# Kernel optimization log

Measured on AMD Instinct MI355X. Metric: run time of the kernel, lower is better.

The kernel has to match this reference:

```python
import jax, jax.numpy as jnp
import numpy as np

B, C, T = 2, 32, 7680
IN_CAPS = 122240  # ((7680-9+1)//4 - 9 + 1) * 2 * 32
OUT_CAPS, OUT_DIM, IN_DIM = 16, 16, 8
ROUTINGS = 3
DN = ('NCHW', 'OIHW', 'NCHW')


def squash(s, axis=-1):
    norm = jnp.linalg.norm(s, axis=axis, keepdims=True)
    scale = norm ** 2 / (1.0 + norm ** 2) / (norm + 1e-8)
    return scale * s


def setup_inputs() -> dict:
    key = jax.random.key(0)
    ks = jax.random.split(key, 9)
    return {
        'x': jax.random.normal(ks[0], (B, C, T), jnp.float32),
        'W_lin': jax.random.normal(ks[1], (C, C), jnp.float32) * 0.1,
        'b_lin': jnp.zeros((C,), jnp.float32),
        'W_conv1': jax.random.normal(ks[2], (16, 1, 1, 9), jnp.float32) * 0.1,
        'b_conv1': jnp.zeros((16,), jnp.float32),
        'W_conv2': jax.random.normal(ks[3], (16, 16, 1, 9), jnp.float32) * 0.05,
        'b_conv2': jnp.zeros((16,), jnp.float32),
        'W_caps': jax.random.normal(ks[4], (OUT_CAPS, IN_CAPS, OUT_DIM, IN_DIM), jnp.float32) * 0.01,
        'W_fc': jax.random.normal(ks[5], (1, 16, 16), jnp.float32) * 0.1,
        'b_fc': jnp.zeros((1,), jnp.float32),
    }


def reference(x, W_lin, b_lin, W_conv1, b_conv1, W_conv2, b_conv2, W_caps, W_fc, b_fc):
    # channel attention: shared linear applied to max-pool and avg-pool over time
    mx = x.max(axis=-1)                      # [B, C]
    av = x.mean(axis=-1)                     # [B, C]
    attn = jax.nn.sigmoid((mx @ W_lin.T + b_lin) + (av @ W_lin.T + b_lin))
    x = x * attn[:, :, None]                 # [B, C, T]

    # conv_first: Conv2d(1,16,(1,9),stride=(1,2)) + ELU + AvgPool2d((1,2),(1,2))
    h = x[:, None, :, :]                     # [B, 1, C, T]
    h = jax.lax.conv_general_dilated(h, W_conv1, (1, 2), 'VALID', dimension_numbers=DN)
    h = jax.nn.elu(h + b_conv1[None, :, None, None])   # [B, 16, 32, 3836]
    b_, ch, hh, ww = h.shape
    h = h[..., : (ww // 2) * 2].reshape(b_, ch, hh, ww // 2, 2).mean(-1)  # [B,16,32,1918]

    # primary capsules: Conv2d(16,16,(1,9)) -> reshape to [B, IN_CAPS, 8] -> squash
    h = jax.lax.conv_general_dilated(h, W_conv2, (1, 1), 'VALID', dimension_numbers=DN)
    h = h + b_conv2[None, :, None, None]     # [B, 16, 32, 1910]
    u = squash(h.reshape(b_, -1, IN_DIM))    # [B, 122240, 8]

    # dense capsule: x_hat[b,j,n,p] = sum_d W_caps[j,n,p,d] * u[b,n,d]
    x_hat = jnp.einsum('jnpd,bnd->bjnp', W_caps, u)  # [B, 16, 122240, 16]
    x_hat_det = jax.lax.stop_gradient(x_hat)
    b_logits = jnp.zeros((b_, OUT_CAPS, IN_CAPS), x_hat.dtype)
    v = None
    for i in range(ROUTINGS):
        c = jax.nn.softmax(b_logits, axis=1)             # [B, 16, 122240]
        xh = x_hat if i == ROUTINGS - 1 else x_hat_det
        v = squash(jnp.einsum('bjn,bjnp->bjp', c, xh))   # [B, 16, 16]
        if i < ROUTINGS - 1:
            b_logits = b_logits + jnp.einsum('bjp,bjnp->bjn', v, x_hat_det)

    # fc: Conv1d(16, 1, 16) over [B, 16, 16] -> [B, 1, 1] -> sigmoid -> squeeze
    out = jax.nn.sigmoid(jnp.einsum('bct,oct->bo', v, W_fc) + b_fc)
    return jnp.squeeze(out)                  # [B]
```

## Files before the change

### kernel.cpp

```cpp
#include <hip/hip_runtime.h>
#include <math.h>

#define IN_CAPS 122240
#define T_LEN   7680
#define PW      1918
#define HW      1910

#define OFF_MX    0
#define OFF_AV    64
#define OFF_ATTN  128
#define OFF_S0    192
#define OFF_S1    704
#define OFF_S2    1216
#define OFF_V0    1728
#define OFF_VSUM  2240
#define OFF_P     2816
#define OFF_H     1966848
#define OFF_U     3922688
#define OFF_XHAT  5878528

__global__ void k_rowstat(const float* __restrict__ x, float* __restrict__ ws) {
    int row = blockIdx.x;
    const float* xr = x + (size_t)row * T_LEN;
    float mx = -INFINITY, sm = 0.f;
    for (int i = threadIdx.x; i < T_LEN; i += 256) {
        float v = xr[i];
        mx = fmaxf(mx, v);
        sm += v;
    }
    __shared__ float smx[256], ssm[256];
    smx[threadIdx.x] = mx; ssm[threadIdx.x] = sm;
    __syncthreads();
    for (int s = 128; s > 0; s >>= 1) {
        if (threadIdx.x < s) {
            smx[threadIdx.x] = fmaxf(smx[threadIdx.x], smx[threadIdx.x + s]);
            ssm[threadIdx.x] += ssm[threadIdx.x + s];
        }
        __syncthreads();
    }
    if (threadIdx.x == 0) {
        ws[OFF_MX + row] = smx[0];
        ws[OFF_AV + row] = ssm[0] * (1.f / (float)T_LEN);
    }
}

__global__ void k_attn_zero(const float* __restrict__ Wl, const float* __restrict__ bl,
                            float* __restrict__ ws) {
    int t = threadIdx.x;
    for (int i = t; i < 1536; i += 256) ws[OFF_S0 + i] = 0.f;
    if (t < 64) {
        int b = t >> 5, c = t & 31;
        float acc = 2.f * bl[c];
        for (int k = 0; k < 32; k++)
            acc += (ws[OFF_MX + b * 32 + k] + ws[OFF_AV + b * 32 + k]) * Wl[c * 32 + k];
        ws[OFF_ATTN + t] = 1.f / (1.f + expf(-acc));
    }
}

__global__ void k_conv1pool(const float* __restrict__ x, const float* __restrict__ w1,
                            const float* __restrict__ b1, float* __restrict__ ws) {
    int idx = blockIdx.x * 256 + threadIdx.x;
    int w2 = idx % PW;
    int hh = (idx / PW) & 31;
    int oc = (idx / (PW * 32)) & 15;
    int b  = idx / (PW * 32 * 16);
    float a = ws[OFF_ATTN + b * 32 + hh];
    const float* xr = x + ((size_t)b * 32 + hh) * T_LEN + 4 * w2;
    const float* wk = w1 + oc * 9;
    float xv[11];
    #pragma unroll
    for (int k = 0; k < 11; k++) xv[k] = xr[k] * a;
    float o0 = 0.f, o1 = 0.f;
    #pragma unroll
    for (int k = 0; k < 9; k++) { o0 += wk[k] * xv[k]; o1 += wk[k] * xv[k + 2]; }
    o0 += b1[oc]; o1 += b1[oc];
    o0 = o0 > 0.f ? o0 : expm1f(o0);
    o1 = o1 > 0.f ? o1 : expm1f(o1);
    ws[OFF_P + idx] = 0.5f * (o0 + o1);
}

__global__ void k_conv2(const float* __restrict__ w2, const float* __restrict__ b2,
                        float* __restrict__ ws) {
    int idx = blockIdx.x * 256 + threadIdx.x;
    int w3 = idx % HW;
    int hh = (idx / HW) & 31;
    int oc = (idx / (HW * 32)) & 15;
    int b  = idx / (HW * 32 * 16);
    float acc = b2[oc];
    const float* wrow = w2 + oc * 144;
    const float* pb = ws + OFF_P + (size_t)b * 16 * 32 * PW + hh * PW + w3;
    #pragma unroll 4
    for (int ic = 0; ic < 16; ic++) {
        const float* pr = pb + (size_t)ic * 32 * PW;
        #pragma unroll
        for (int k = 0; k < 9; k++) acc += wrow[ic * 9 + k] * pr[k];
    }
    ws[OFF_H + idx] = acc;
}

__global__ void k_squash_u(float* __restrict__ ws) {
    int n = blockIdx.x * 256 + threadIdx.x;
    const float4* hp = (const float4*)(ws + OFF_H) + (size_t)n * 2;
    float4 a = hp[0], b = hp[1];
    float ns = a.x*a.x + a.y*a.y + a.z*a.z + a.w*a.w
             + b.x*b.x + b.y*b.y + b.z*b.z + b.w*b.w;
    float nrm = sqrtf(ns);
    float scale = ns / (1.f + ns) / (nrm + 1e-8f);
    a.x *= scale; a.y *= scale; a.z *= scale; a.w *= scale;
    b.x *= scale; b.y *= scale; b.z *= scale; b.w *= scale;
    float4* up = (float4*)(ws + OFF_U) + (size_t)n * 2;
    up[0] = a; up[1] = b;
}

__global__ void __launch_bounds__(256) k_xhat(const float* __restrict__ Wc,
                                              float* __restrict__ ws) {
    const int j = threadIdx.x >> 4;
    const int p = threadIdx.x & 15;
    const int n0 = blockIdx.x * 128;
    const float* u = ws + OFF_U;
    float* xhat = ws + OFF_XHAT;
    const size_t wbase = (size_t)j * IN_CAPS * 128 + (size_t)p * 8;
    float sum0 = 0.f, sum1 = 0.f;
    for (int k = 0; k < 128; k++) {
        const int n = n0 + k;
        const float4* wp = (const float4*)(Wc + wbase + (size_t)n * 128);
        float4 wa = wp[0], wb = wp[1];
        const float4* ua = (const float4*)(u + ((size_t)n << 3));
        const float4* ub = (const float4*)(u + ((size_t)(IN_CAPS + n) << 3));
        float4 a0 = ua[0], a1 = ua[1];
        float4 c0 = ub[0], c1 = ub[1];
        float xh0 = wa.x*a0.x + wa.y*a0.y + wa.z*a0.z + wa.w*a0.w
                  + wb.x*a1.x + wb.y*a1.y + wb.z*a1.z + wb.w*a1.w;
        float xh1 = wa.x*c0.x + wa.y*c0.y + wa.z*c0.z + wa.w*c0.w
                  + wb.x*c1.x + wb.y*c1.y + wb.z*c1.z + wb.w*c1.w;
        xhat[((size_t)n << 8) + (j << 4) + p] = xh0;
        xhat[((size_t)(IN_CAPS + n) << 8) + (j << 4) + p] = xh1;
        sum0 += xh0; sum1 += xh1;
    }
    atomicAdd(&ws[OFF_S0 + (j << 4) + p], sum0);
    atomicAdd(&ws[OFF_S0 + 256 + (j << 4) + p], sum1);
}

__global__ void __launch_bounds__(256) k_route(const float* __restrict__ xhat,
                                               const float* __restrict__ vin,
                                               float* __restrict__ sout,
                                               int nwaves_per_b) {
    const int tid = threadIdx.x;
    const int wid = tid >> 6;
    const int lane = tid & 63;
    const int j = lane >> 2;
    const int pq = lane & 3;
    const int b = wid & 1;
    __shared__ float vsh[512];
    for (int i = tid; i < 512; i += 256) vsh[i] = vin[i];
    __syncthreads();
    const float* vp = &vsh[(((b << 4) + j) << 4) + (pq << 2)];
    const float v0 = vp[0], v1 = vp[1], v2 = vp[2], v3 = vp[3];
    const int wb = (blockIdx.x << 1) + (wid >> 1);
    const float* xb = xhat + (size_t)b * IN_CAPS * 256;
    float4 acc = make_float4(0.f, 0.f, 0.f, 0.f);
    for (int n = wb; n < IN_CAPS; n += nwaves_per_b) {
        float4 xh = *(const float4*)(xb + ((size_t)n << 8) + (j << 4) + (pq << 2));
        float t = v0 * xh.x + v1 * xh.y + v2 * xh.z + v3 * xh.w;
        t += __shfl_xor(t, 1);
        t += __shfl_xor(t, 2);
        float tmax = t;
        tmax = fmaxf(tmax, __shfl_xor(tmax, 4));
        tmax = fmaxf(tmax, __shfl_xor(tmax, 8));
        tmax = fmaxf(tmax, __shfl_xor(tmax, 16));
        tmax = fmaxf(tmax, __shfl_xor(tmax, 32));
        float e = expf(t - tmax);
        float es = e;
        es += __shfl_xor(es, 4);
        es += __shfl_xor(es, 8);
        es += __shfl_xor(es, 16);
        es += __shfl_xor(es, 32);
        float c = e / es;
        acc.x += c * xh.x; acc.y += c * xh.y; acc.z += c * xh.z; acc.w += c * xh.w;
    }
    __shared__ float4 accsh[4][64];
    accsh[wid][lane] = acc;
    __syncthreads();
    if (tid < 128) {
        float4 a = accsh[wid][lane];
        float4 c = accsh[wid + 2][lane];
        float* dst = sout + (((wid << 4) + j) << 4) + (pq << 2);
        atomicAdd(dst + 0, a.x + c.x);
        atomicAdd(dst + 1, a.y + c.y);
        atomicAdd(dst + 2, a.z + c.z);
        atomicAdd(dst + 3, a.w + c.w);
    }
}

__global__ void __launch_bounds__(512) k_vstep(float* __restrict__ ws,
                                               const float* __restrict__ wfc,
                                               const float* __restrict__ bfc,
                                               float* __restrict__ out,
                                               int mode) {
    __shared__ float sv[512];
    const int t = threadIdx.x;
    int soff = (mode == 0) ? OFF_S0 : (mode == 1) ? OFF_S1 : OFF_S2;
    float val = ws[soff + t];
    if (mode == 0) val *= (1.f / 16.f);
    sv[t] = val;
    __syncthreads();
    const int bj = t >> 4;
    float ns = 0.f;
    #pragma unroll
    for (int p = 0; p < 16; p++) { float q = sv[(bj << 4) + p]; ns += q * q; }
    float nrm = sqrtf(ns);
    float scale = ns / (1.f + ns) / (nrm + 1e-8f);
    float v = scale * val;
    if (mode == 0) {
        ws[OFF_V0 + t] = v;
    } else if (mode == 1) {
        ws[OFF_VSUM + t] = ws[OFF_V0 + t] + v;
    } else {
        __syncthreads();
        sv[t] = v * wfc[t & 255];
        __syncthreads();
        for (int s = 128; s > 0; s >>= 1) {
            if ((t & 255) < s) sv[t] += sv[t + s];
            __syncthreads();
        }
        if ((t & 255) == 0)
            out[t >> 8] = 1.f / (1.f + expf(-(sv[t] + bfc[0])));
    }
}

extern "C" void kernel_launch(void* const* d_in, const int* in_sizes, int n_in,
                              void* d_out, int out_size, void* d_ws, size_t ws_size,
                              hipStream_t stream) {
    const float* x   = (const float*)d_in[0];
    const float* Wl  = (const float*)d_in[1];
    const float* bl  = (const float*)d_in[2];
    const float* W1  = (const float*)d_in[3];
    const float* b1  = (const float*)d_in[4];
    const float* W2  = (const float*)d_in[5];
    const float* b2  = (const float*)d_in[6];
    const float* Wc  = (const float*)d_in[7];
    const float* Wfc = (const float*)d_in[8];
    const float* bfc = (const float*)d_in[9];
    float* out = (float*)d_out;
    float* ws  = (float*)d_ws;

    k_rowstat  <<<64, 256, 0, stream>>>(x, ws);
    k_attn_zero<<<1, 256, 0, stream>>>(Wl, bl, ws);
    k_conv1pool<<<7672, 256, 0, stream>>>(x, W1, b1, ws);
    k_conv2    <<<7640, 256, 0, stream>>>(W2, b2, ws);
    k_squash_u <<<955, 256, 0, stream>>>(ws);
    k_xhat     <<<955, 256, 0, stream>>>(Wc, ws);
    k_vstep    <<<1, 512, 0, stream>>>(ws, Wfc, bfc, out, 0);
    k_route    <<<256, 256, 0, stream>>>(ws + OFF_XHAT, ws + OFF_V0, ws + OFF_S1, 512);
    k_vstep    <<<1, 512, 0, stream>>>(ws, Wfc, bfc, out, 1);
    k_route    <<<256, 256, 0, stream>>>(ws + OFF_XHAT, ws + OFF_VSUM, ws + OFF_S2, 512);
    k_vstep    <<<1, 512, 0, stream>>>(ws, Wfc, bfc, out, 2);
}
```

Before: 1.806 ms.

## Store x_hat in bf16 and restructure routing to one capsule per thread group

x_hat is now written as bf16 in the dense-capsule kernel and read back as bf16 in both routing passes, halving the bytes of the largest intermediate (about 500 MB in fp32). The routing kernel is rewritten so each group of 4 threads handles all 16 output capsules of one input capsule. The softmax over j then runs in registers instead of through cross-lane shuffles, and results are reduced once at the end with one atomic per output element. This costs precision in x_hat (bf16 rounding of the routing inputs) and adds register pressure from the 16 float4 accumulators.

```diff
diff --git a/kernel.cpp b/kernel.cpp
--- a/kernel.cpp
+++ b/kernel.cpp
@@ -1,4 +1,5 @@
 #include <hip/hip_runtime.h>
+#include <hip/hip_bf16.h>
 #include <math.h>
 
 #define IN_CAPS 122240
@@ -18,6 +19,15 @@
 #define OFF_H     1966848
 #define OFF_U     3922688
 #define OFF_XHAT  5878528
+
+__device__ __forceinline__ float4 bf4_to_f4(ushort4 r) {
+    float4 o;
+    o.x = __uint_as_float(((unsigned)r.x) << 16);
+    o.y = __uint_as_float(((unsigned)r.y) << 16);
+    o.z = __uint_as_float(((unsigned)r.z) << 16);
+    o.w = __uint_as_float(((unsigned)r.w) << 16);
+    return o;
+}
 
 __global__ void k_rowstat(const float* __restrict__ x, float* __restrict__ ws) {
     int row = blockIdx.x;
@@ -118,9 +128,10 @@
     const int p = threadIdx.x & 15;
     const int n0 = blockIdx.x * 128;
     const float* u = ws + OFF_U;
-    float* xhat = ws + OFF_XHAT;
+    __hip_bfloat16* xhat = (__hip_bfloat16*)(ws + OFF_XHAT);
     const size_t wbase = (size_t)j * IN_CAPS * 128 + (size_t)p * 8;
     float sum0 = 0.f, sum1 = 0.f;
+    #pragma unroll 2
     for (int k = 0; k < 128; k++) {
         const int n = n0 + k;
         const float4* wp = (const float4*)(Wc + wbase + (size_t)n * 128);
@@ -133,63 +144,85 @@
                   + wb.x*a1.x + wb.y*a1.y + wb.z*a1.z + wb.w*a1.w;
         float xh1 = wa.x*c0.x + wa.y*c0.y + wa.z*c0.z + wa.w*c0.w
                   + wb.x*c1.x + wb.y*c1.y + wb.z*c1.z + wb.w*c1.w;
-        xhat[((size_t)n << 8) + (j << 4) + p] = xh0;
-        xhat[((size_t)(IN_CAPS + n) << 8) + (j << 4) + p] = xh1;
+        xhat[((size_t)n << 8) + (j << 4) + p] = __float2bfloat16(xh0);
+        xhat[((size_t)(IN_CAPS + n) << 8) + (j << 4) + p] = __float2bfloat16(xh1);
         sum0 += xh0; sum1 += xh1;
     }
     atomicAdd(&ws[OFF_S0 + (j << 4) + p], sum0);
     atomicAdd(&ws[OFF_S0 + 256 + (j << 4) + p], sum1);
 }
 
-__global__ void __launch_bounds__(256) k_route(const float* __restrict__ xhat,
+__global__ void __launch_bounds__(256) k_route(const ushort* __restrict__ xhat,
                                                const float* __restrict__ vin,
-                                               float* __restrict__ sout,
-                                               int nwaves_per_b) {
+                                               float* __restrict__ sout) {
     const int tid = threadIdx.x;
+    const int lane = tid & 63;
     const int wid = tid >> 6;
-    const int lane = tid & 63;
-    const int j = lane >> 2;
-    const int pq = lane & 3;
-    const int b = wid & 1;
-    __shared__ float vsh[512];
-    for (int i = tid; i < 512; i += 256) vsh[i] = vin[i];
-    __syncthreads();
-    const float* vp = &vsh[(((b << 4) + j) << 4) + (pq << 2)];
-    const float v0 = vp[0], v1 = vp[1], v2 = vp[2], v3 = vp[3];
-    const int wb = (blockIdx.x << 1) + (wid >> 1);
-    const float* xb = xhat + (size_t)b * IN_CAPS * 256;
-    float4 acc = make_float4(0.f, 0.f, 0.f, 0.f);
-    for (int n = wb; n < IN_CAPS; n += nwaves_per_b) {
-        float4 xh = *(const float4*)(xb + ((size_t)n << 8) + (j << 4) + (pq << 2));
-        float t = v0 * xh.x + v1 * xh.y + v2 * xh.z + v3 * xh.w;
-        t += __shfl_xor(t, 1);
-        t += __shfl_xor(t, 2);
-        float tmax = t;
-        tmax = fmaxf(tmax, __shfl_xor(tmax, 4));
-        tmax = fmaxf(tmax, __shfl_xor(tmax, 8));
-        tmax = fmaxf(tmax, __shfl_xor(tmax, 16));
-        tmax = fmaxf(tmax, __shfl_xor(tmax, 32));
-        float e = expf(t - tmax);
-        float es = e;
-        es += __shfl_xor(es, 4);
-        es += __shfl_xor(es, 8);
-        es += __shfl_xor(es, 16);
-        es += __shfl_xor(es, 32);
-        float c = e / es;
-        acc.x += c * xh.x; acc.y += c * xh.y; acc.z += c * xh.z; acc.w += c * xh.w;
-    }
-    __shared__ float4 accsh[4][64];
-    accsh[wid][lane] = acc;
-    __syncthreads();
-    if (tid < 128) {
-        float4 a = accsh[wid][lane];
-        float4 c = accsh[wid + 2][lane];
-        float* dst = sout + (((wid << 4) + j) << 4) + (pq << 2);
-        atomicAdd(dst + 0, a.x + c.x);
-        atomicAdd(dst + 1, a.y + c.y);
-        atomicAdd(dst + 2, a.z + c.z);
-        atomicAdd(dst + 3, a.w + c.w);
-    }
+    const int q = tid & 3;
+    const int b = blockIdx.x & 1;
+    __shared__ float vsh[256];
+    __shared__ float red[4][256];
+    vsh[tid] = vin[(b << 8) + tid];
+    __syncthreads();
+
+    const int g_global = ((blockIdx.x >> 1) << 6) + (tid >> 2);
+    const ushort* xb = xhat + ((size_t)b * IN_CAPS << 8);
+    float4 acc[16];
+    #pragma unroll
+    for (int j = 0; j < 16; j++) acc[j] = make_float4(0.f, 0.f, 0.f, 0.f);
+
+    for (int k = 0; k < 8; k++) {
+        const int n = g_global + (k << 14);
+        if (n < IN_CAPS) {
+            const ushort* base = xb + ((size_t)n << 8) + (q << 2);
+            ushort4 raw[16];
+            float t[16];
+            #pragma unroll
+            for (int j = 0; j < 16; j++) {
+                raw[j] = *(const ushort4*)(base + (j << 4));
+                float4 xf = bf4_to_f4(raw[j]);
+                float4 vv = *(const float4*)&vsh[(j << 4) + (q << 2)];
+                t[j] = vv.x*xf.x + vv.y*xf.y + vv.z*xf.z + vv.w*xf.w;
+            }
+            #pragma unroll
+            for (int j = 0; j < 16; j++) {
+                t[j] += __shfl_xor(t[j], 1);
+                t[j] += __shfl_xor(t[j], 2);
+            }
+            float tmax = t[0];
+            #pragma unroll
+            for (int j = 1; j < 16; j++) tmax = fmaxf(tmax, t[j]);
+            float e[16]; float es = 0.f;
+            #pragma unroll
+            for (int j = 0; j < 16; j++) { e[j] = __expf(t[j] - tmax); es += e[j]; }
+            float inv = 1.f / es;
+            #pragma unroll
+            for (int j = 0; j < 16; j++) {
+                float c = e[j] * inv;
+                float4 xf = bf4_to_f4(raw[j]);
+                acc[j].x += c * xf.x; acc[j].y += c * xf.y;
+                acc[j].z += c * xf.z; acc[j].w += c * xf.w;
+            }
+        }
+    }
+    #pragma unroll
+    for (int j = 0; j < 16; j++) {
+        #pragma unroll
+        for (int m = 4; m < 64; m <<= 1) {
+            acc[j].x += __shfl_xor(acc[j].x, m);
+            acc[j].y += __shfl_xor(acc[j].y, m);
+            acc[j].z += __shfl_xor(acc[j].z, m);
+            acc[j].w += __shfl_xor(acc[j].w, m);
+        }
+    }
+    if (lane < 4) {
+        #pragma unroll
+        for (int j = 0; j < 16; j++)
+            *(float4*)&red[wid][(j << 4) + (lane << 2)] = acc[j];
+    }
+    __syncthreads();
+    float s = red[0][tid] + red[1][tid] + red[2][tid] + red[3][tid];
+    atomicAdd(&sout[(b << 8) + tid], s);
 }
 
 __global__ void __launch_bounds__(512) k_vstep(float* __restrict__ ws,
@@ -243,6 +276,7 @@
     const float* bfc = (const float*)d_in[9];
     float* out = (float*)d_out;
     float* ws  = (float*)d_ws;
+    const ushort* xh16 = (const ushort*)(ws + OFF_XHAT);
 
     k_rowstat  <<<64, 256, 0, stream>>>(x, ws);
     k_attn_zero<<<1, 256, 0, stream>>>(Wl, bl, ws);
@@ -251,8 +285,8 @@
     k_squash_u <<<955, 256, 0, stream>>>(ws);
     k_xhat     <<<955, 256, 0, stream>>>(Wc, ws);
     k_vstep    <<<1, 512, 0, stream>>>(ws, Wfc, bfc, out, 0);
-    k_route    <<<256, 256, 0, stream>>>(ws + OFF_XHAT, ws + OFF_V0, ws + OFF_S1, 512);
+    k_route    <<<512, 256, 0, stream>>>(xh16, ws + OFF_V0, ws + OFF_S1);
     k_vstep    <<<1, 512, 0, stream>>>(ws, Wfc, bfc, out, 1);
-    k_route    <<<256, 256, 0, stream>>>(ws + OFF_XHAT, ws + OFF_VSUM, ws + OFF_S2, 512);
+    k_route    <<<512, 256, 0, stream>>>(xh16, ws + OFF_VSUM, ws + OFF_S2);
     k_vstep    <<<1, 512, 0, stream>>>(ws, Wfc, bfc, out, 2);
 }
```

Measured after the change: 1.462 ms. 1.24x faster.
